# Performance work log

Measured on AMD Instinct MI355X. Metric: run time of the kernel, lower is better.

Reference implementation:

```python
import jax, jax.numpy as jnp
import numpy as np

N, E, IN, H, G, OUT = 50000, 800000, 128, 128, 64, 10
HEADS, C = 4, 32  # per-head dim = H // HEADS so 4-head concat -> H (keeps chain dims consistent)


def setup_inputs() -> dict:
    key = jax.random.key(0)
    ks = jax.random.split(key, 16)
    p = lambda i, shape: jax.random.normal(ks[i], shape, jnp.float32) * 0.05
    return {
        "x": jax.random.normal(ks[0], (N, IN), jnp.float32),
        "edge_index": jax.random.randint(ks[1], (2, E), 0, N),
        "batch": jnp.sort(jax.random.randint(ks[2], (N,), 0, G)),
        "gcn_W": p(3, (IN, H)), "gcn_b": jnp.zeros((H,), jnp.float32),
        "gat_W": p(4, (H, HEADS * C)),
        "att_src": p(5, (HEADS, C)), "att_dst": p(6, (HEADS, C)),
        "gat_b": jnp.zeros((HEADS * C,), jnp.float32),
        "ec_W1": p(7, (2 * H, 128)), "ec_b1": jnp.zeros((128,), jnp.float32),
        "ec_W2": p(8, (128, H)), "ec_b2": jnp.zeros((H,), jnp.float32),
        "gin_W1": p(9, (H, 128)), "gin_b1": jnp.zeros((128,), jnp.float32),
        "gin_W2": p(10, (128, H)), "gin_b2": jnp.zeros((H,), jnp.float32),
        "gate_W1": p(11, (H, 128)), "gate_b1": jnp.zeros((128,), jnp.float32),
        "gate_W2": p(12, (128, 1)), "gate_b2": jnp.zeros((1,), jnp.float32),
        "fc_W": p(13, (H, OUT)), "fc_b": jnp.zeros((OUT,), jnp.float32),
    }


def reference(x, edge_index, batch, gcn_W, gcn_b, gat_W, att_src, att_dst, gat_b,
              ec_W1, ec_b1, ec_W2, ec_b2, gin_W1, gin_b1, gin_W2, gin_b2,
              gate_W1, gate_b1, gate_W2, gate_b2, fc_W, fc_b):
    src, dst = edge_index[0], edge_index[1]
    loop = jnp.arange(N)
    src_l = jnp.concatenate([src, loop])  # self loops for GCN / GAT
    dst_l = jnp.concatenate([dst, loop])

    deg = jax.ops.segment_sum(jnp.ones_like(dst_l, jnp.float32), dst_l, N)
    dinv = jnp.where(deg > 0, jax.lax.rsqrt(deg), 0.0)
    h = x @ gcn_W
    norm = dinv[src_l] * dinv[dst_l]  # [E+N]
    h = jax.ops.segment_sum(h[src_l] * norm[:, None], dst_l, N) + gcn_b
    h = jax.nn.relu(h)

    # ---- GATConv: 4 heads, per-target edge softmax, concat ----
    g = (h @ gat_W).reshape(N, HEADS, C)
    a_src = (g * att_src).sum(-1)  # [N, HEADS]
    a_dst = (g * att_dst).sum(-1)
    e = jax.nn.leaky_relu(a_src[src_l] + a_dst[dst_l], 0.2)  # [E+N, HEADS]
    e_max = jax.ops.segment_max(e, dst_l, N)
    e = jnp.exp(e - e_max[dst_l])
    e_sum = jax.ops.segment_sum(e, dst_l, N)
    alpha = e / (e_sum[dst_l] + 1e-16)
    h = jax.ops.segment_sum(g[src_l] * alpha[..., None], dst_l, N).reshape(N, HEADS * C) + gat_b
    h = jax.nn.elu(h)

    # ---- EdgeConv: nn([x_i, x_j - x_i]) with max aggregation ----
    msg = jnp.concatenate([h[dst], h[src] - h[dst]], axis=-1)  # [E, 2H]
    msg = jax.nn.relu(msg @ ec_W1 + ec_b1) @ ec_W2 + ec_b2
    agg = jax.ops.segment_max(msg, dst, N)
    h = jax.nn.relu(jnp.where(jnp.isfinite(agg), agg, 0.0))  # isolated nodes -> 0 (PyG scatter-max fill)

    # ---- GINConv (eps=0): nn(x + sum_j x_j) ----
    s = h + jax.ops.segment_sum(h[src], dst, N)
    h = jax.nn.relu(jax.nn.relu(s @ gin_W1 + gin_b1) @ gin_W2 + gin_b2)

    # ---- GlobalAttention pooling: per-graph softmax gating ----
    gate = jax.nn.relu(h @ gate_W1 + gate_b1) @ gate_W2 + gate_b2  # [N, 1]
    gmax = jax.ops.segment_max(gate, batch, G)
    ge = jnp.exp(gate - gmax[batch])
    gsum = jax.ops.segment_sum(ge, batch, G)
    w = ge / (gsum[batch] + 1e-16)
    pooled = jax.ops.segment_sum(w * h, batch, G)  # [G, H]

    out = pooled @ fc_W + fc_b
    return jax.nn.log_softmax(out, axis=1)
```

## Files before the change

### kernel.cpp

```cpp
#include <hip/hip_runtime.h>

#define H 128
#define OUTD 10

typedef short bf16x8 __attribute__((ext_vector_type(8)));
typedef float f32x4 __attribute__((ext_vector_type(4)));

__device__ __forceinline__ unsigned short f2bf(float x) {
  unsigned u = __float_as_uint(x);
  u += 0x7fffu + ((u >> 16) & 1u);
  return (unsigned short)(u >> 16);
}
__device__ __forceinline__ unsigned pack2bf(float a, float b) {
  return (unsigned)f2bf(a) | ((unsigned)f2bf(b) << 16);
}
__device__ __forceinline__ float bf2f(unsigned short u) {
  return __uint_as_float(((unsigned)u) << 16);
}
__device__ __forceinline__ float bflo(unsigned u) { return __uint_as_float(u << 16); }
__device__ __forceinline__ float bfhi(unsigned u) { return __uint_as_float(u & 0xffff0000u); }

__global__ void prep_w(const float* __restrict__ gcnW, const float* __restrict__ gatW,
                       const float* __restrict__ ecW1, const float* __restrict__ ecW2,
                       const float* __restrict__ ginW1, const float* __restrict__ ginW2,
                       const float* __restrict__ gtW1, unsigned short* __restrict__ WT) {
  int f = blockIdx.x * 256 + threadIdx.x;
  if (f >= 8 * 16384) return;
  int m = f >> 14, idx = f & 16383;
  int j = idx >> 7, k = idx & 127;
  int src = k * 128 + j;
  float v;
  switch (m) {
    case 0: v = gcnW[src]; break;
    case 1: v = gatW[src]; break;
    case 2: v = ecW1[src] - ecW1[16384 + src]; break;
    case 3: v = ecW1[16384 + src]; break;
    case 4: v = ecW2[src]; break;
    case 5: v = ginW1[src]; break;
    case 6: v = ginW2[src]; break;
    default: v = gtW1[src]; break;
  }
  WT[f] = f2bf(v);
}

template <int IN_BF, int RELU, int BIAS>
__global__ __launch_bounds__(256) void dense_mfma(const void* __restrict__ Xv,
                                                  const unsigned short* __restrict__ WT,
                                                  const float* __restrict__ bias,
                                                  unsigned short* __restrict__ Y, int n) {
  __shared__ unsigned short tile[64][136];
  const int tid = threadIdx.x, lane = tid & 63, wave = tid >> 6;
  const int jl = lane & 15, kg = lane >> 4;
  const int base = blockIdx.x * 64;
  if (base >= n) return;
  const int nr = min(64, n - base);
  if (IN_BF) {
    const uint4* X4 = (const uint4*)Xv;
#pragma unroll
    for (int it = 0; it < 4; ++it) {
      int f = it * 256 + tid, r = f >> 4, q = f & 15;
      if (r < nr) *(uint4*)&tile[r][q * 8] = X4[(size_t)(base + r) * 16 + q];
    }
  } else {
    const float* X = (const float*)Xv;
#pragma unroll
    for (int it = 0; it < 16; ++it) {
      int f = it * 256 + tid, r = f >> 6, kp = f & 63;
      if (r < nr) {
        float2 v = *(const float2*)&X[(size_t)(base + r) * H + 2 * kp];
        *(unsigned*)&tile[r][2 * kp] = pack2bf(v.x, v.y);
      }
    }
  }
  __syncthreads();
  bf16x8 afrag[4];
#pragma unroll
  for (int kk = 0; kk < 4; ++kk)
    afrag[kk] = *(const bf16x8*)&tile[wave * 16 + jl][kk * 32 + kg * 8];
  f32x4 acc[8];
#pragma unroll
  for (int jt = 0; jt < 8; ++jt) {
    f32x4 c = {0.f, 0.f, 0.f, 0.f};
#pragma unroll
    for (int kk = 0; kk < 4; ++kk) {
      bf16x8 bf = *(const bf16x8*)&WT[(size_t)(jt * 16 + jl) * H + kk * 32 + kg * 8];
      c = __builtin_amdgcn_mfma_f32_16x16x32_bf16(afrag[kk], bf, c, 0, 0, 0);
    }
    if (BIAS) {
      float bb = bias[jt * 16 + jl];
#pragma unroll
      for (int r = 0; r < 4; ++r) c[r] += bb;
    }
    if (RELU) {
#pragma unroll
      for (int r = 0; r < 4; ++r) c[r] = fmaxf(c[r], 0.f);
    }
    acc[jt] = c;
  }
  __syncthreads();
#pragma unroll
  for (int jt = 0; jt < 8; ++jt)
#pragma unroll
    for (int r = 0; r < 4; ++r) tile[wave * 16 + kg * 4 + r][jt * 16 + jl] = f2bf(acc[jt][r]);
  __syncthreads();
#pragma unroll
  for (int it = 0; it < 4; ++it) {
    int f = it * 256 + tid, r = f >> 4, q = f & 15;
    if (r < nr) *(uint4*)&Y[(size_t)(base + r) * H + q * 8] = *(const uint4*)&tile[r][q * 8];
  }
}

__global__ __launch_bounds__(256) void dense_dual(const unsigned short* __restrict__ X,
                                                  const unsigned short* __restrict__ WT1,
                                                  const unsigned short* __restrict__ WT2,
                                                  const float* __restrict__ bias2,
                                                  unsigned short* __restrict__ Y1,
                                                  unsigned short* __restrict__ Y2, int n) {
  __shared__ unsigned short tile[64][136];
  const int tid = threadIdx.x, lane = tid & 63, wave = tid >> 6;
  const int jl = lane & 15, kg = lane >> 4;
  const int base = blockIdx.x * 64;
  if (base >= n) return;
  const int nr = min(64, n - base);
  const uint4* X4 = (const uint4*)X;
#pragma unroll
  for (int it = 0; it < 4; ++it) {
    int f = it * 256 + tid, r = f >> 4, q = f & 15;
    if (r < nr) *(uint4*)&tile[r][q * 8] = X4[(size_t)(base + r) * 16 + q];
  }
  __syncthreads();
  bf16x8 afrag[4];
#pragma unroll
  for (int kk = 0; kk < 4; ++kk)
    afrag[kk] = *(const bf16x8*)&tile[wave * 16 + jl][kk * 32 + kg * 8];
  f32x4 acc[8];
#pragma unroll
  for (int jt = 0; jt < 8; ++jt) {
    f32x4 c = {0.f, 0.f, 0.f, 0.f};
#pragma unroll
    for (int kk = 0; kk < 4; ++kk) {
      bf16x8 bf = *(const bf16x8*)&WT1[(size_t)(jt * 16 + jl) * H + kk * 32 + kg * 8];
      c = __builtin_amdgcn_mfma_f32_16x16x32_bf16(afrag[kk], bf, c, 0, 0, 0);
    }
    acc[jt] = c;
  }
  __syncthreads();
#pragma unroll
  for (int jt = 0; jt < 8; ++jt)
#pragma unroll
    for (int r = 0; r < 4; ++r) tile[wave * 16 + kg * 4 + r][jt * 16 + jl] = f2bf(acc[jt][r]);
  __syncthreads();
#pragma unroll
  for (int it = 0; it < 4; ++it) {
    int f = it * 256 + tid, r = f >> 4, q = f & 15;
    if (r < nr) *(uint4*)&Y1[(size_t)(base + r) * H + q * 8] = *(const uint4*)&tile[r][q * 8];
  }
  __syncthreads();
#pragma unroll
  for (int jt = 0; jt < 8; ++jt) {
    f32x4 c = {0.f, 0.f, 0.f, 0.f};
#pragma unroll
    for (int kk = 0; kk < 4; ++kk) {
      bf16x8 bf = *(const bf16x8*)&WT2[(size_t)(jt * 16 + jl) * H + kk * 32 + kg * 8];
      c = __builtin_amdgcn_mfma_f32_16x16x32_bf16(afrag[kk], bf, c, 0, 0, 0);
    }
    float bb = bias2[jt * 16 + jl];
#pragma unroll
    for (int r = 0; r < 4; ++r) c[r] += bb;
    acc[jt] = c;
  }
  __syncthreads();
#pragma unroll
  for (int jt = 0; jt < 8; ++jt)
#pragma unroll
    for (int r = 0; r < 4; ++r) tile[wave * 16 + kg * 4 + r][jt * 16 + jl] = f2bf(acc[jt][r]);
  __syncthreads();
#pragma unroll
  for (int it = 0; it < 4; ++it) {
    int f = it * 256 + tid, r = f >> 4, q = f & 15;
    if (r < nr) *(uint4*)&Y2[(size_t)(base + r) * H + q * 8] = *(const uint4*)&tile[r][q * 8];
  }
}

__global__ void zero_int(int* p, int n) {
  int i = blockIdx.x * 256 + threadIdx.x;
  if (i < n) p[i] = 0;
}
__global__ void csr_count(const int* __restrict__ ei, int* __restrict__ cnt, int E) {
  int e = blockIdx.x * 256 + threadIdx.x;
  if (e < E) atomicAdd(&cnt[ei[(size_t)E + e]], 1);
}
__global__ __launch_bounds__(1024) void scan50k(const int* __restrict__ cnt,
                                                int* __restrict__ row_ptr, int n) {
  __shared__ int ls[1024];
  int t = threadIdx.x;
  int chunk = (n + 1023) >> 10;
  int a = t * chunk;
  if (a > n) a = n;
  int b = a + chunk;
  if (b > n) b = n;
  int s = 0;
  for (int i = a; i < b; ++i) s += cnt[i];
  ls[t] = s;
  __syncthreads();
  for (int off = 1; off < 1024; off <<= 1) {
    int v = (t >= off) ? ls[t - off] : 0;
    __syncthreads();
    ls[t] += v;
    __syncthreads();
  }
  int run = (t > 0) ? ls[t - 1] : 0;
  for (int i = a; i < b; ++i) {
    row_ptr[i] = run;
    run += cnt[i];
  }
  if (t == 1023) row_ptr[n] = ls[1023];
}
__global__ void copy_int(const int* __restrict__ a, int* __restrict__ b, int n) {
  int i = blockIdx.x * 256 + threadIdx.x;
  if (i < n) b[i] = a[i];
}
__global__ void csr_fill(const int* __restrict__ ei, int* __restrict__ cursor,
                         int* __restrict__ csr_src, int E) {
  int e = blockIdx.x * 256 + threadIdx.x;
  if (e >= E) return;
  int s = ei[e], d = ei[(size_t)E + e];
  int p = atomicAdd(&cursor[d], 1);
  csr_src[p] = s;
}
__global__ void dinv_kernel(const int* __restrict__ row_ptr, float* __restrict__ dinv, int n) {
  int i = blockIdx.x * 256 + threadIdx.x;
  if (i < n) dinv[i] = rsqrtf((float)(1 + row_ptr[i + 1] - row_ptr[i]));
}

__global__ __launch_bounds__(256) void gcn_gather(const unsigned short* __restrict__ h,
                                                  const float* __restrict__ dinv,
                                                  const int* __restrict__ row_ptr,
                                                  const int* __restrict__ csr_src,
                                                  const float* __restrict__ bias,
                                                  unsigned short* __restrict__ out, int n) {
  int node = blockIdx.x * 4 + (threadIdx.x >> 6);
  int lane = threadIdx.x & 63;
  if (node >= n) return;
  const unsigned* hu = (const unsigned*)h;
  float di = dinv[node];
  unsigned v = hu[(size_t)node * 64 + lane];
  float t0 = bflo(v) * di, t1 = bfhi(v) * di;
  int a = row_ptr[node], b = row_ptr[node + 1];
  int e = a;
  for (; e + 4 <= b; e += 4) {
    int s0 = csr_src[e], s1 = csr_src[e + 1], s2 = csr_src[e + 2], s3 = csr_src[e + 3];
    unsigned w0 = hu[(size_t)s0 * 64 + lane], w1 = hu[(size_t)s1 * 64 + lane];
    unsigned w2 = hu[(size_t)s2 * 64 + lane], w3 = hu[(size_t)s3 * 64 + lane];
    float d0 = dinv[s0], d1 = dinv[s1], d2 = dinv[s2], d3 = dinv[s3];
    t0 = fmaf(bflo(w0), d0, t0);
    t1 = fmaf(bfhi(w0), d0, t1);
    t0 = fmaf(bflo(w1), d1, t0);
    t1 = fmaf(bfhi(w1), d1, t1);
    t0 = fmaf(bflo(w2), d2, t0);
    t1 = fmaf(bfhi(w2), d2, t1);
    t0 = fmaf(bflo(w3), d3, t0);
    t1 = fmaf(bfhi(w3), d3, t1);
  }
  for (; e < b; ++e) {
    int s = csr_src[e];
    float ds = dinv[s];
    unsigned w = hu[(size_t)s * 64 + lane];
    t0 = fmaf(bflo(w), ds, t0);
    t1 = fmaf(bfhi(w), ds, t1);
  }
  float y0 = fmaxf(fmaf(t0, di, bias[lane * 2]), 0.f);
  float y1 = fmaxf(fmaf(t1, di, bias[lane * 2 + 1]), 0.f);
  ((unsigned*)out)[(size_t)node * 64 + lane] = pack2bf(y0, y1);
}

__global__ void att_pre(const unsigned short* __restrict__ g, const float* __restrict__ attS,
                        const float* __restrict__ attD, float* __restrict__ asrc,
                        float* __restrict__ adst, int n) {
  int t = blockIdx.x * 256 + threadIdx.x;
  if (t >= n * 4) return;
  int i = t >> 2, hd = t & 3;
  const unsigned* gr = (const unsigned*)(g + (size_t)i * H + hd * 32);
  float s1 = 0.f, s2 = 0.f;
#pragma unroll
  for (int p = 0; p < 16; ++p) {
    unsigned u = gr[p];
    float a = bflo(u), b = bfhi(u);
    s1 = fmaf(a, attS[hd * 32 + 2 * p], fmaf(b, attS[hd * 32 + 2 * p + 1], s1));
    s2 = fmaf(a, attD[hd * 32 + 2 * p], fmaf(b, attD[hd * 32 + 2 * p + 1], s2));
  }
  asrc[t] = s1;
  adst[t] = s2;
}

__device__ __forceinline__ float lrelu_exp(float v) {
  v = v > 0.f ? v : 0.2f * v;
  return __expf(v);
}

__global__ __launch_bounds__(256) void gat_gather(const unsigned short* __restrict__ g,
                                                  const float* __restrict__ asrc,
                                                  const float* __restrict__ adst,
                                                  const int* __restrict__ row_ptr,
                                                  const int* __restrict__ csr_src,
                                                  const float* __restrict__ bias,
                                                  unsigned short* __restrict__ out, int n) {
  int node = blockIdx.x * 4 + (threadIdx.x >> 6);
  int lane = threadIdx.x & 63;
  if (node >= n) return;
  const int hd = lane >> 4;
  const unsigned* gu = (const unsigned*)g;
  float adc = adst[node * 4 + hd];
  float w = lrelu_exp(asrc[node * 4 + hd] + adc);
  unsigned u = gu[(size_t)node * 64 + lane];
  float acc0 = w * bflo(u), acc1 = w * bfhi(u), wsum = w;
  int a = row_ptr[node], b = row_ptr[node + 1];
  int e = a;
  for (; e + 4 <= b; e += 4) {
    int s0 = csr_src[e], s1 = csr_src[e + 1], s2 = csr_src[e + 2], s3 = csr_src[e + 3];
    unsigned u0 = gu[(size_t)s0 * 64 + lane], u1 = gu[(size_t)s1 * 64 + lane];
    unsigned u2 = gu[(size_t)s2 * 64 + lane], u3 = gu[(size_t)s3 * 64 + lane];
    float w0 = lrelu_exp(asrc[s0 * 4 + hd] + adc), w1 = lrelu_exp(asrc[s1 * 4 + hd] + adc);
    float w2 = lrelu_exp(asrc[s2 * 4 + hd] + adc), w3 = lrelu_exp(asrc[s3 * 4 + hd] + adc);
    acc0 = fmaf(w0, bflo(u0), acc0);
    acc1 = fmaf(w0, bfhi(u0), acc1);
    acc0 = fmaf(w1, bflo(u1), acc0);
    acc1 = fmaf(w1, bfhi(u1), acc1);
    acc0 = fmaf(w2, bflo(u2), acc0);
    acc1 = fmaf(w2, bfhi(u2), acc1);
    acc0 = fmaf(w3, bflo(u3), acc0);
    acc1 = fmaf(w3, bfhi(u3), acc1);
    wsum += w0 + w1 + w2 + w3;
  }
  for (; e < b; ++e) {
    int s = csr_src[e];
    unsigned us = gu[(size_t)s * 64 + lane];
    float we = lrelu_exp(asrc[s * 4 + hd] + adc);
    acc0 = fmaf(we, bflo(us), acc0);
    acc1 = fmaf(we, bfhi(us), acc1);
    wsum += we;
  }
  float inv = 1.f / (wsum + 1e-16f);
  float r0 = acc0 * inv + bias[2 * lane];
  float r1 = acc1 * inv + bias[2 * lane + 1];
  r0 = r0 > 0.f ? r0 : expm1f(r0);
  r1 = r1 > 0.f ? r1 : expm1f(r1);
  ((unsigned*)out)[(size_t)node * 64 + lane] = pack2bf(r0, r1);
}

__global__ __launch_bounds__(256) void edgeconv_node(const unsigned short* __restrict__ A,
                                                     const unsigned short* __restrict__ Bm,
                                                     const int* __restrict__ row_ptr,
                                                     const int* __restrict__ csr_src,
                                                     const unsigned short* __restrict__ W2T,
                                                     const float* __restrict__ b2,
                                                     unsigned short* __restrict__ out, int n) {
  int node = blockIdx.x * 4 + (threadIdx.x >> 6);
  if (node >= n) return;
  const int lane = threadIdx.x & 63;
  const int jl = lane & 15, kg = lane >> 4;
  int a = row_ptr[node], b = row_ptr[node + 1];
  unsigned* orow = (unsigned*)(out + (size_t)node * H);
  if (a == b) {
    if (kg == 0 && !(jl & 1)) {
#pragma unroll
      for (int jt = 0; jt < 8; ++jt) orow[jt * 8 + (jl >> 1)] = 0u;
    }
    return;
  }
  bf16x8 ad[4];
  const unsigned short* Arow = A + (size_t)node * H;
#pragma unroll
  for (int kk = 0; kk < 4; ++kk) ad[kk] = *(const bf16x8*)&Arow[kk * 32 + kg * 8];
  f32x4 best[8];
#pragma unroll
  for (int jt = 0; jt < 8; ++jt) best[jt] = {-1e30f, -1e30f, -1e30f, -1e30f};
  for (int base = a; base < b; base += 16) {
    const int m = min(16, b - base);
    bf16x8 af[4];
    if (jl < m) {
      int s = csr_src[base + jl];
      const unsigned short* Brow = Bm + (size_t)s * H;
#pragma unroll
      for (int kk = 0; kk < 4; ++kk) {
        bf16x8 bv = *(const bf16x8*)&Brow[kk * 32 + kg * 8];
        bf16x8 o;
#pragma unroll
        for (int q = 0; q < 8; ++q) {
          float xv = bf2f((unsigned short)ad[kk][q]) + bf2f((unsigned short)bv[q]);
          o[q] = (short)f2bf(fmaxf(xv, 0.f));
        }
        af[kk] = o;
      }
    } else {
#pragma unroll
      for (int kk = 0; kk < 4; ++kk) {
#pragma unroll
        for (int q = 0; q < 8; ++q) af[kk][q] = 0;
      }
    }
#pragma unroll
    for (int jt = 0; jt < 8; ++jt) {
      f32x4 c = {0.f, 0.f, 0.f, 0.f};
#pragma unroll
      for (int kk = 0; kk < 4; ++kk) {
        bf16x8 wf = *(const bf16x8*)&W2T[(size_t)(jt * 16 + jl) * H + kk * 32 + kg * 8];
        c = __builtin_amdgcn_mfma_f32_16x16x32_bf16(af[kk], wf, c, 0, 0, 0);
      }
#pragma unroll
      for (int r = 0; r < 4; ++r) {
        int row = kg * 4 + r;
        best[jt][r] = fmaxf(best[jt][r], (row < m) ? c[r] : -1e30f);
      }
    }
  }
#pragma unroll
  for (int jt = 0; jt < 8; ++jt) {
    float mv = fmaxf(fmaxf(best[jt][0], best[jt][1]), fmaxf(best[jt][2], best[jt][3]));
    mv = fmaxf(mv, __shfl_xor(mv, 16));
    mv = fmaxf(mv, __shfl_xor(mv, 32));
    float val = fmaxf(mv + b2[jt * 16 + jl], 0.f);
    float other = __shfl_xor(val, 1);
    if (kg == 0 && !(jl & 1)) orow[jt * 8 + (jl >> 1)] = pack2bf(val, other);
  }
}

__global__ __launch_bounds__(256) void gin_gather(const unsigned short* __restrict__ h,
                                                  const int* __restrict__ row_ptr,
                                                  const int* __restrict__ csr_src,
                                                  unsigned short* __restrict__ out, int n) {
  int node = blockIdx.x * 4 + (threadIdx.x >> 6);
  int lane = threadIdx.x & 63;
  if (node >= n) return;
  const unsigned* hu = (const unsigned*)h;
  unsigned v = hu[(size_t)node * 64 + lane];
  float t0 = bflo(v), t1 = bfhi(v);
  int a = row_ptr[node], b = row_ptr[node + 1];
  int e = a;
  for (; e + 4 <= b; e += 4) {
    int s0 = csr_src[e], s1 = csr_src[e + 1], s2 = csr_src[e + 2], s3 = csr_src[e + 3];
    unsigned w0 = hu[(size_t)s0 * 64 + lane], w1 = hu[(size_t)s1 * 64 + lane];
    unsigned w2 = hu[(size_t)s2 * 64 + lane], w3 = hu[(size_t)s3 * 64 + lane];
    t0 += bflo(w0) + bflo(w1) + bflo(w2) + bflo(w3);
    t1 += bfhi(w0) + bfhi(w1) + bfhi(w2) + bfhi(w3);
  }
  for (; e < b; ++e) {
    int s = csr_src[e];
    unsigned w = hu[(size_t)s * 64 + lane];
    t0 += bflo(w);
    t1 += bfhi(w);
  }
  ((unsigned*)out)[(size_t)node * 64 + lane] = pack2bf(t0, t1);
}

__global__ __launch_bounds__(256) void gate_dot(const unsigned short* __restrict__ X,
                                                const float* __restrict__ w2,
                                                const float* __restrict__ b2,
                                                float* __restrict__ gate, int n) {
  int wid = (blockIdx.x * 256 + threadIdx.x) >> 6;
  int lane = threadIdx.x & 63;
  if (wid >= n) return;
  unsigned u = ((const unsigned*)X)[(size_t)wid * 64 + lane];
  float a = fmaf(bflo(u), w2[lane * 2], bfhi(u) * w2[lane * 2 + 1]);
#pragma unroll
  for (int off = 32; off; off >>= 1) a += __shfl_xor(a, off);
  if (lane == 0) gate[wid] = a + b2[0];
}
__global__ void starts_kernel(const int* __restrict__ batch, int* __restrict__ starts, int n,
                              int G) {
  int i = blockIdx.x * 256 + threadIdx.x;
  if (i >= n) return;
  int b = batch[i];
  int bp = (i == 0) ? -1 : batch[i - 1];
  for (int g = bp + 1; g <= b; ++g) starts[g] = i;
  if (i == n - 1)
    for (int g = b + 1; g <= G; ++g) starts[g] = n;
}
__global__ __launch_bounds__(256) void pool_fused(float* __restrict__ gate,
                                                  const unsigned short* __restrict__ h4,
                                                  const int* __restrict__ starts,
                                                  const float* __restrict__ fcW,
                                                  const float* __restrict__ fcB,
                                                  float* __restrict__ out) {
  __shared__ float red[256];
  __shared__ float pl[128];
  int g = blockIdx.x, t = threadIdx.x;
  int s0 = starts[g], s1 = starts[g + 1];
  float m = -1e30f;
  for (int i = s0 + t; i < s1; i += 256) m = fmaxf(m, gate[i]);
  red[t] = m;
  __syncthreads();
  for (int off = 128; off; off >>= 1) {
    if (t < off) red[t] = fmaxf(red[t], red[t + off]);
    __syncthreads();
  }
  m = red[0];
  __syncthreads();
  float sm = 0.f;
  for (int i = s0 + t; i < s1; i += 256) {
    float ge = __expf(gate[i] - m);
    gate[i] = ge;
    sm += ge;
  }
  red[t] = sm;
  __syncthreads();
  for (int off = 128; off; off >>= 1) {
    if (t < off) red[t] += red[t + off];
    __syncthreads();
  }
  float inv = 1.f / (red[0] + 1e-16f);
  __syncthreads();
  int c = t & 127, half = t >> 7;
  float acc = 0.f;
  for (int i = s0 + half; i < s1; i += 2) acc = fmaf(gate[i], bf2f(h4[(size_t)i * H + c]), acc);
  red[t] = acc;
  __syncthreads();
  if (t < 128) pl[t] = (red[t] + red[t + 128]) * inv;
  __syncthreads();
  if (t < OUTD) {
    float o = fcB[t];
    for (int k = 0; k < 128; ++k) o = fmaf(pl[k], fcW[k * OUTD + t], o);
    red[t] = o;
  }
  __syncthreads();
  if (t == 0) {
    float mm = -1e30f;
    for (int j = 0; j < OUTD; ++j) mm = fmaxf(mm, red[j]);
    float s = 0.f;
    for (int j = 0; j < OUTD; ++j) s += __expf(red[j] - mm);
    float l = logf(s);
    for (int j = 0; j < OUTD; ++j) out[g * OUTD + j] = red[j] - mm - l;
  }
}

extern "C" void kernel_launch(void* const* d_in, const int* in_sizes, int n_in, void* d_out,
                              int out_size, void* d_ws, size_t ws_size, hipStream_t stream) {
  const float* x = (const float*)d_in[0];
  const int* ei = (const int*)d_in[1];
  const int* batch = (const int*)d_in[2];
  const float* gcnW = (const float*)d_in[3];
  const float* gcnB = (const float*)d_in[4];
  const float* gatW = (const float*)d_in[5];
  const float* attS = (const float*)d_in[6];
  const float* attD = (const float*)d_in[7];
  const float* gatB = (const float*)d_in[8];
  const float* ecW1 = (const float*)d_in[9];
  const float* ecB1 = (const float*)d_in[10];
  const float* ecW2 = (const float*)d_in[11];
  const float* ecB2 = (const float*)d_in[12];
  const float* ginW1 = (const float*)d_in[13];
  const float* ginB1 = (const float*)d_in[14];
  const float* ginW2 = (const float*)d_in[15];
  const float* ginB2 = (const float*)d_in[16];
  const float* gtW1 = (const float*)d_in[17];
  const float* gtB1 = (const float*)d_in[18];
  const float* gtW2 = (const float*)d_in[19];
  const float* gtB2 = (const float*)d_in[20];
  const float* fcW = (const float*)d_in[21];
  const float* fcB = (const float*)d_in[22];

  const int N = in_sizes[0] / H;
  const int E = in_sizes[1] / 2;
  const int G = out_size / OUTD;
  const size_t NH = (size_t)N * H;

  auto align16 = [](char* p) { return (char*)(((uintptr_t)p + 15) & ~(uintptr_t)15); };
  char* p = (char*)d_ws;
  float* dinv = (float*)p;           p += (size_t)N * 4;
  float* asrc = (float*)p;           p += (size_t)4 * N * 4;
  float* adst = (float*)p;           p += (size_t)4 * N * 4;
  float* gate = (float*)p;           p += (size_t)N * 4;
  int* starts = (int*)p;             p += (size_t)(G + 1) * 4;
  int* cnt = (int*)p;                p += (size_t)N * 4;
  int* row_ptr = (int*)p;            p += (size_t)(N + 1) * 4;
  int* cursor = (int*)p;             p += (size_t)N * 4;
  int* csr_src = (int*)p;            p += (size_t)E * 4;
  p = align16(p);
  unsigned short* WT = (unsigned short*)p;  p += (size_t)8 * 16384 * 2;
  p = align16(p);
  unsigned short* T0 = (unsigned short*)p;  p += NH * 2;
  p = align16(p);
  unsigned short* T1 = (unsigned short*)p;  p += NH * 2;
  p = align16(p);
  unsigned short* T2 = (unsigned short*)p;  p += NH * 2;
  p = align16(p);
  unsigned short* T3 = (unsigned short*)p;  p += NH * 2;

  const unsigned short* gcnT = WT;
  const unsigned short* gatT = WT + 16384;
  const unsigned short* WaT = WT + 2 * 16384;
  const unsigned short* WbT = WT + 3 * 16384;
  const unsigned short* W2T = WT + 4 * 16384;
  const unsigned short* gin1T = WT + 5 * 16384;
  const unsigned short* gin2T = WT + 6 * 16384;
  const unsigned short* gt1T = WT + 7 * 16384;

  const int gN = (N + 255) / 256;
  const int gE = (E + 255) / 256;
  const int gDense = (N + 63) / 64;
  const int gW4 = (N + 3) / 4;

  prep_w<<<(8 * 16384 + 255) / 256, 256, 0, stream>>>(gcnW, gatW, ecW1, ecW2, ginW1, ginW2,
                                                      gtW1, WT);
  zero_int<<<gN, 256, 0, stream>>>(cnt, N);
  csr_count<<<gE, 256, 0, stream>>>(ei, cnt, E);
  scan50k<<<1, 1024, 0, stream>>>(cnt, row_ptr, N);
  copy_int<<<gN, 256, 0, stream>>>(row_ptr, cursor, N);
  csr_fill<<<gE, 256, 0, stream>>>(ei, cursor, csr_src, E);
  dinv_kernel<<<gN, 256, 0, stream>>>(row_ptr, dinv, N);

  dense_mfma<0, 0, 0><<<gDense, 256, 0, stream>>>(x, gcnT, nullptr, T0, N);
  gcn_gather<<<gW4, 256, 0, stream>>>(T0, dinv, row_ptr, csr_src, gcnB, T1, N);

  dense_mfma<1, 0, 0><<<gDense, 256, 0, stream>>>(T1, gatT, nullptr, T2, N);
  att_pre<<<(N * 4 + 255) / 256, 256, 0, stream>>>(T2, attS, attD, asrc, adst, N);
  gat_gather<<<gW4, 256, 0, stream>>>(T2, asrc, adst, row_ptr, csr_src, gatB, T0, N);

  dense_dual<<<gDense, 256, 0, stream>>>(T0, WaT, WbT, ecB1, T1, T2, N);
  edgeconv_node<<<gW4, 256, 0, stream>>>(T1, T2, row_ptr, csr_src, W2T, ecB2, T3, N);

  gin_gather<<<gW4, 256, 0, stream>>>(T3, row_ptr, csr_src, T0, N);
  dense_mfma<1, 1, 1><<<gDense, 256, 0, stream>>>(T0, gin1T, ginB1, T1, N);
  dense_mfma<1, 1, 1><<<gDense, 256, 0, stream>>>(T1, gin2T, ginB2, T2, N);

  dense_mfma<1, 1, 1><<<gDense, 256, 0, stream>>>(T2, gt1T, gtB1, T0, N);
  gate_dot<<<(N * 64 + 255) / 256, 256, 0, stream>>>(T0, gtW2, gtB2, gate, N);
  starts_kernel<<<gN, 256, 0, stream>>>(batch, starts, N, G);
  pool_fused<<<G, 256, 0, stream>>>(gate, T2, starts, fcW, fcB, (float*)d_out);
}
```

Baseline: 976.0 us.

## Edge-tiled EdgeConv with atomic max, fuse GIN MLP and gate head

EdgeConv changes from per-node wave processing, which leaves MFMA tiles partly idle for low-degree nodes, to dense 64-edge tiles in CSR order. Tiles are double-buffered in a persistent grid, and results are merged with atomicMax on an order-preserving uint32 encoding into an fp32 buffer. The GIN two-layer MLP is fused into one kernel, and the gate's first layer is fused with its dot product. The GCN gather is also unrolled to 8 edges. The cost is extra atomic traffic, a fill pass, a csr_dst array and a wider fp32 intermediate. Isolated nodes now decode the fill value to 0, so the output should match the reference.

Result: faster. 817.0 us (-16.3%).

```diff
diff --git a/kernel.cpp b/kernel.cpp
--- a/kernel.cpp
+++ b/kernel.cpp
@@ -19,6 +19,15 @@
 }
 __device__ __forceinline__ float bflo(unsigned u) { return __uint_as_float(u << 16); }
 __device__ __forceinline__ float bfhi(unsigned u) { return __uint_as_float(u & 0xffff0000u); }
+
+__device__ __forceinline__ unsigned fenc(float x) {
+  unsigned u = __float_as_uint(x);
+  return (u & 0x80000000u) ? ~u : (u | 0x80000000u);
+}
+__device__ __forceinline__ float fdec(unsigned u) {
+  u = (u & 0x80000000u) ? (u & 0x7fffffffu) : ~u;
+  return __uint_as_float(u);
+}
 
 __global__ void prep_w(const float* __restrict__ gcnW, const float* __restrict__ gatW,
                        const float* __restrict__ ecW1, const float* __restrict__ ecW2,
@@ -182,6 +191,131 @@
   }
 }
 
+__global__ __launch_bounds__(256) void dense_chain(const unsigned short* __restrict__ X,
+                                                   const unsigned short* __restrict__ WT1,
+                                                   const float* __restrict__ b1,
+                                                   const unsigned short* __restrict__ WT2,
+                                                   const float* __restrict__ b2,
+                                                   unsigned short* __restrict__ Y, int n) {
+  __shared__ unsigned short tile[64][136];
+  const int tid = threadIdx.x, lane = tid & 63, wave = tid >> 6;
+  const int jl = lane & 15, kg = lane >> 4;
+  const int base = blockIdx.x * 64;
+  if (base >= n) return;
+  const int nr = min(64, n - base);
+  const uint4* X4 = (const uint4*)X;
+#pragma unroll
+  for (int it = 0; it < 4; ++it) {
+    int f = it * 256 + tid, r = f >> 4, q = f & 15;
+    if (r < nr) *(uint4*)&tile[r][q * 8] = X4[(size_t)(base + r) * 16 + q];
+  }
+  __syncthreads();
+  bf16x8 af[4];
+#pragma unroll
+  for (int kk = 0; kk < 4; ++kk) af[kk] = *(const bf16x8*)&tile[wave * 16 + jl][kk * 32 + kg * 8];
+  f32x4 acc[8];
+#pragma unroll
+  for (int jt = 0; jt < 8; ++jt) {
+    f32x4 c = {0.f, 0.f, 0.f, 0.f};
+#pragma unroll
+    for (int kk = 0; kk < 4; ++kk) {
+      bf16x8 bf = *(const bf16x8*)&WT1[(size_t)(jt * 16 + jl) * H + kk * 32 + kg * 8];
+      c = __builtin_amdgcn_mfma_f32_16x16x32_bf16(af[kk], bf, c, 0, 0, 0);
+    }
+    float bb = b1[jt * 16 + jl];
+#pragma unroll
+    for (int r = 0; r < 4; ++r) c[r] = fmaxf(c[r] + bb, 0.f);
+    acc[jt] = c;
+  }
+  __syncthreads();
+#pragma unroll
+  for (int jt = 0; jt < 8; ++jt)
+#pragma unroll
+    for (int r = 0; r < 4; ++r) tile[wave * 16 + kg * 4 + r][jt * 16 + jl] = f2bf(acc[jt][r]);
+  __syncthreads();
+#pragma unroll
+  for (int kk = 0; kk < 4; ++kk) af[kk] = *(const bf16x8*)&tile[wave * 16 + jl][kk * 32 + kg * 8];
+#pragma unroll
+  for (int jt = 0; jt < 8; ++jt) {
+    f32x4 c = {0.f, 0.f, 0.f, 0.f};
+#pragma unroll
+    for (int kk = 0; kk < 4; ++kk) {
+      bf16x8 bf = *(const bf16x8*)&WT2[(size_t)(jt * 16 + jl) * H + kk * 32 + kg * 8];
+      c = __builtin_amdgcn_mfma_f32_16x16x32_bf16(af[kk], bf, c, 0, 0, 0);
+    }
+    float bb = b2[jt * 16 + jl];
+#pragma unroll
+    for (int r = 0; r < 4; ++r) c[r] = fmaxf(c[r] + bb, 0.f);
+    acc[jt] = c;
+  }
+  __syncthreads();
+#pragma unroll
+  for (int jt = 0; jt < 8; ++jt)
+#pragma unroll
+    for (int r = 0; r < 4; ++r) tile[wave * 16 + kg * 4 + r][jt * 16 + jl] = f2bf(acc[jt][r]);
+  __syncthreads();
+#pragma unroll
+  for (int it = 0; it < 4; ++it) {
+    int f = it * 256 + tid, r = f >> 4, q = f & 15;
+    if (r < nr) *(uint4*)&Y[(size_t)(base + r) * H + q * 8] = *(const uint4*)&tile[r][q * 8];
+  }
+}
+
+__global__ __launch_bounds__(256) void dense_gate(const unsigned short* __restrict__ X,
+                                                  const unsigned short* __restrict__ WT,
+                                                  const float* __restrict__ b1,
+                                                  const float* __restrict__ w2,
+                                                  const float* __restrict__ b2,
+                                                  float* __restrict__ gate, int n) {
+  __shared__ unsigned short tile[64][136];
+  const int tid = threadIdx.x, lane = tid & 63, wave = tid >> 6;
+  const int jl = lane & 15, kg = lane >> 4;
+  const int base = blockIdx.x * 64;
+  if (base >= n) return;
+  const int nr = min(64, n - base);
+  const uint4* X4 = (const uint4*)X;
+#pragma unroll
+  for (int it = 0; it < 4; ++it) {
+    int f = it * 256 + tid, r = f >> 4, q = f & 15;
+    if (r < nr) *(uint4*)&tile[r][q * 8] = X4[(size_t)(base + r) * 16 + q];
+  }
+  __syncthreads();
+  bf16x8 af[4];
+#pragma unroll
+  for (int kk = 0; kk < 4; ++kk) af[kk] = *(const bf16x8*)&tile[wave * 16 + jl][kk * 32 + kg * 8];
+  float p0 = 0.f, p1 = 0.f, p2 = 0.f, p3 = 0.f;
+#pragma unroll
+  for (int jt = 0; jt < 8; ++jt) {
+    f32x4 c = {0.f, 0.f, 0.f, 0.f};
+#pragma unroll
+    for (int kk = 0; kk < 4; ++kk) {
+      bf16x8 bf = *(const bf16x8*)&WT[(size_t)(jt * 16 + jl) * H + kk * 32 + kg * 8];
+      c = __builtin_amdgcn_mfma_f32_16x16x32_bf16(af[kk], bf, c, 0, 0, 0);
+    }
+    float bb = b1[jt * 16 + jl];
+    float wv = w2[jt * 16 + jl];
+    p0 = fmaf(fmaxf(c[0] + bb, 0.f), wv, p0);
+    p1 = fmaf(fmaxf(c[1] + bb, 0.f), wv, p1);
+    p2 = fmaf(fmaxf(c[2] + bb, 0.f), wv, p2);
+    p3 = fmaf(fmaxf(c[3] + bb, 0.f), wv, p3);
+  }
+#pragma unroll
+  for (int off = 1; off <= 8; off <<= 1) {
+    p0 += __shfl_xor(p0, off);
+    p1 += __shfl_xor(p1, off);
+    p2 += __shfl_xor(p2, off);
+    p3 += __shfl_xor(p3, off);
+  }
+  if (jl == 0) {
+    float bb2 = b2[0];
+    int row = wave * 16 + kg * 4;
+    if (row + 0 < nr) gate[base + row + 0] = p0 + bb2;
+    if (row + 1 < nr) gate[base + row + 1] = p1 + bb2;
+    if (row + 2 < nr) gate[base + row + 2] = p2 + bb2;
+    if (row + 3 < nr) gate[base + row + 3] = p3 + bb2;
+  }
+}
+
 __global__ void zero_int(int* p, int n) {
   int i = blockIdx.x * 256 + threadIdx.x;
   if (i < n) p[i] = 0;
@@ -221,16 +355,21 @@
   if (i < n) b[i] = a[i];
 }
 __global__ void csr_fill(const int* __restrict__ ei, int* __restrict__ cursor,
-                         int* __restrict__ csr_src, int E) {
+                         int* __restrict__ csr_src, int* __restrict__ csr_dst, int E) {
   int e = blockIdx.x * 256 + threadIdx.x;
   if (e >= E) return;
   int s = ei[e], d = ei[(size_t)E + e];
   int p = atomicAdd(&cursor[d], 1);
   csr_src[p] = s;
+  csr_dst[p] = d;
 }
 __global__ void dinv_kernel(const int* __restrict__ row_ptr, float* __restrict__ dinv, int n) {
   int i = blockIdx.x * 256 + threadIdx.x;
   if (i < n) dinv[i] = rsqrtf((float)(1 + row_ptr[i + 1] - row_ptr[i]));
+}
+__global__ void fill_u32(unsigned* p, unsigned v, size_t n) {
+  size_t i = (size_t)blockIdx.x * 256 + threadIdx.x;
+  if (i < n) p[i] = v;
 }
 
 __global__ __launch_bounds__(256) void gcn_gather(const unsigned short* __restrict__ h,
@@ -248,19 +387,21 @@
   float t0 = bflo(v) * di, t1 = bfhi(v) * di;
   int a = row_ptr[node], b = row_ptr[node + 1];
   int e = a;
-  for (; e + 4 <= b; e += 4) {
-    int s0 = csr_src[e], s1 = csr_src[e + 1], s2 = csr_src[e + 2], s3 = csr_src[e + 3];
-    unsigned w0 = hu[(size_t)s0 * 64 + lane], w1 = hu[(size_t)s1 * 64 + lane];
-    unsigned w2 = hu[(size_t)s2 * 64 + lane], w3 = hu[(size_t)s3 * 64 + lane];
-    float d0 = dinv[s0], d1 = dinv[s1], d2 = dinv[s2], d3 = dinv[s3];
-    t0 = fmaf(bflo(w0), d0, t0);
-    t1 = fmaf(bfhi(w0), d0, t1);
-    t0 = fmaf(bflo(w1), d1, t0);
-    t1 = fmaf(bfhi(w1), d1, t1);
-    t0 = fmaf(bflo(w2), d2, t0);
-    t1 = fmaf(bfhi(w2), d2, t1);
-    t0 = fmaf(bflo(w3), d3, t0);
-    t1 = fmaf(bfhi(w3), d3, t1);
+  for (; e + 8 <= b; e += 8) {
+    int sx[8];
+#pragma unroll
+    for (int i = 0; i < 8; ++i) sx[i] = csr_src[e + i];
+    unsigned w[8];
+    float dd[8];
+#pragma unroll
+    for (int i = 0; i < 8; ++i) w[i] = hu[(size_t)sx[i] * 64 + lane];
+#pragma unroll
+    for (int i = 0; i < 8; ++i) dd[i] = dinv[sx[i]];
+#pragma unroll
+    for (int i = 0; i < 8; ++i) {
+      t0 = fmaf(bflo(w[i]), dd[i], t0);
+      t1 = fmaf(bfhi(w[i]), dd[i], t1);
+    }
   }
   for (; e < b; ++e) {
     int s = csr_src[e];
@@ -348,57 +489,81 @@
   ((unsigned*)out)[(size_t)node * 64 + lane] = pack2bf(r0, r1);
 }
 
-__global__ __launch_bounds__(256) void edgeconv_node(const unsigned short* __restrict__ A,
+__global__ __launch_bounds__(256) void edgeconv_tile(const unsigned short* __restrict__ A,
                                                      const unsigned short* __restrict__ Bm,
-                                                     const int* __restrict__ row_ptr,
                                                      const int* __restrict__ csr_src,
+                                                     const int* __restrict__ csr_dst,
                                                      const unsigned short* __restrict__ W2T,
                                                      const float* __restrict__ b2,
-                                                     unsigned short* __restrict__ out, int n) {
-  int node = blockIdx.x * 4 + (threadIdx.x >> 6);
-  if (node >= n) return;
-  const int lane = threadIdx.x & 63;
+                                                     unsigned* __restrict__ hec, int E) {
+  __shared__ unsigned short buf[2][64][136];
+  __shared__ int dbuf[2][64];
+  const int tid = threadIdx.x, lane = tid & 63, wave = tid >> 6;
   const int jl = lane & 15, kg = lane >> 4;
-  int a = row_ptr[node], b = row_ptr[node + 1];
-  unsigned* orow = (unsigned*)(out + (size_t)node * H);
-  if (a == b) {
-    if (kg == 0 && !(jl & 1)) {
-#pragma unroll
-      for (int jt = 0; jt < 8; ++jt) orow[jt * 8 + (jl >> 1)] = 0u;
-    }
-    return;
-  }
-  bf16x8 ad[4];
-  const unsigned short* Arow = A + (size_t)node * H;
-#pragma unroll
-  for (int kk = 0; kk < 4; ++kk) ad[kk] = *(const bf16x8*)&Arow[kk * 32 + kg * 8];
-  f32x4 best[8];
-#pragma unroll
-  for (int jt = 0; jt < 8; ++jt) best[jt] = {-1e30f, -1e30f, -1e30f, -1e30f};
-  for (int base = a; base < b; base += 16) {
-    const int m = min(16, b - base);
-    bf16x8 af[4];
-    if (jl < m) {
-      int s = csr_src[base + jl];
-      const unsigned short* Brow = Bm + (size_t)s * H;
-#pragma unroll
-      for (int kk = 0; kk < 4; ++kk) {
-        bf16x8 bv = *(const bf16x8*)&Brow[kk * 32 + kg * 8];
-        bf16x8 o;
-#pragma unroll
-        for (int q = 0; q < 8; ++q) {
-          float xv = bf2f((unsigned short)ad[kk][q]) + bf2f((unsigned short)bv[q]);
-          o[q] = (short)f2bf(fmaxf(xv, 0.f));
-        }
-        af[kk] = o;
+  const int srow = tid >> 2, sq = tid & 3;
+  float b2v[8];
+#pragma unroll
+  for (int jt = 0; jt < 8; ++jt) b2v[jt] = b2[jt * 16 + jl];
+
+  const int tiles = (E + 63) >> 6;
+  int t = blockIdx.x;
+  if (t >= tiles) return;
+  int cur = 0;
+  {
+    int base = t << 6;
+    int ne = min(64, E - base);
+    uint2 pk[8];
+    if (srow < ne) {
+      int d = csr_dst[base + srow], s = csr_src[base + srow];
+      const uint2* Ar = (const uint2*)(A + (size_t)d * H + sq * 32);
+      const uint2* Br = (const uint2*)(Bm + (size_t)s * H + sq * 32);
+#pragma unroll
+      for (int i = 0; i < 8; ++i) {
+        uint2 va = Ar[i], vb = Br[i];
+        pk[i].x = pack2bf(fmaxf(bflo(va.x) + bflo(vb.x), 0.f), fmaxf(bfhi(va.x) + bfhi(vb.x), 0.f));
+        pk[i].y = pack2bf(fmaxf(bflo(va.y) + bflo(vb.y), 0.f), fmaxf(bfhi(va.y) + bfhi(vb.y), 0.f));
       }
     } else {
 #pragma unroll
-      for (int kk = 0; kk < 4; ++kk) {
-#pragma unroll
-        for (int q = 0; q < 8; ++q) af[kk][q] = 0;
+      for (int i = 0; i < 8; ++i) pk[i] = {0u, 0u};
+    }
+#pragma unroll
+    for (int i = 0; i < 8; ++i) *(uint2*)&buf[0][srow][sq * 32 + i * 4] = pk[i];
+    if (sq == 0) dbuf[0][srow] = (srow < ne) ? csr_dst[base + srow] : -1;
+  }
+  __syncthreads();
+
+  for (; t < tiles; t += gridDim.x) {
+    const int nt = t + gridDim.x;
+    const bool havenext = nt < tiles;
+    uint2 pk[8];
+    if (havenext) {
+      int base = nt << 6;
+      int ne = min(64, E - base);
+      if (srow < ne) {
+        int d = csr_dst[base + srow], s = csr_src[base + srow];
+        const uint2* Ar = (const uint2*)(A + (size_t)d * H + sq * 32);
+        const uint2* Br = (const uint2*)(Bm + (size_t)s * H + sq * 32);
+#pragma unroll
+        for (int i = 0; i < 8; ++i) {
+          uint2 va = Ar[i], vb = Br[i];
+          pk[i].x =
+              pack2bf(fmaxf(bflo(va.x) + bflo(vb.x), 0.f), fmaxf(bfhi(va.x) + bfhi(vb.x), 0.f));
+          pk[i].y =
+              pack2bf(fmaxf(bflo(va.y) + bflo(vb.y), 0.f), fmaxf(bfhi(va.y) + bfhi(vb.y), 0.f));
+        }
+      } else {
+#pragma unroll
+        for (int i = 0; i < 8; ++i) pk[i] = {0u, 0u};
       }
     }
+    bf16x8 af[4];
+#pragma unroll
+    for (int kk = 0; kk < 4; ++kk)
+      af[kk] = *(const bf16x8*)&buf[cur][wave * 16 + jl][kk * 32 + kg * 8];
+    const int r0 = wave * 16 + kg * 4;
+    const int d0 = dbuf[cur][r0 + 0], d1 = dbuf[cur][r0 + 1];
+    const int d2 = dbuf[cur][r0 + 2], d3 = dbuf[cur][r0 + 3];
 #pragma unroll
     for (int jt = 0; jt < 8; ++jt) {
       f32x4 c = {0.f, 0.f, 0.f, 0.f};
@@ -407,65 +572,70 @@
         bf16x8 wf = *(const bf16x8*)&W2T[(size_t)(jt * 16 + jl) * H + kk * 32 + kg * 8];
         c = __builtin_amdgcn_mfma_f32_16x16x32_bf16(af[kk], wf, c, 0, 0, 0);
       }
-#pragma unroll
-      for (int r = 0; r < 4; ++r) {
-        int row = kg * 4 + r;
-        best[jt][r] = fmaxf(best[jt][r], (row < m) ? c[r] : -1e30f);
-      }
-    }
-  }
-#pragma unroll
-  for (int jt = 0; jt < 8; ++jt) {
-    float mv = fmaxf(fmaxf(best[jt][0], best[jt][1]), fmaxf(best[jt][2], best[jt][3]));
-    mv = fmaxf(mv, __shfl_xor(mv, 16));
-    mv = fmaxf(mv, __shfl_xor(mv, 32));
-    float val = fmaxf(mv + b2[jt * 16 + jl], 0.f);
-    float other = __shfl_xor(val, 1);
-    if (kg == 0 && !(jl & 1)) orow[jt * 8 + (jl >> 1)] = pack2bf(val, other);
-  }
-}
-
-__global__ __launch_bounds__(256) void gin_gather(const unsigned short* __restrict__ h,
+      const int col = jt * 16 + jl;
+      int cd = d0;
+      float m = c[0];
+      if (d1 != cd) {
+        if (cd >= 0) atomicMax(&hec[(size_t)cd * H + col], fenc(m + b2v[jt]));
+        cd = d1;
+        m = c[1];
+      } else
+        m = fmaxf(m, c[1]);
+      if (d2 != cd) {
+        if (cd >= 0) atomicMax(&hec[(size_t)cd * H + col], fenc(m + b2v[jt]));
+        cd = d2;
+        m = c[2];
+      } else
+        m = fmaxf(m, c[2]);
+      if (d3 != cd) {
+        if (cd >= 0) atomicMax(&hec[(size_t)cd * H + col], fenc(m + b2v[jt]));
+        cd = d3;
+        m = c[3];
+      } else
+        m = fmaxf(m, c[3]);
+      if (cd >= 0) atomicMax(&hec[(size_t)cd * H + col], fenc(m + b2v[jt]));
+    }
+    if (havenext) {
+      int base = nt << 6;
+      int ne = min(64, E - base);
+#pragma unroll
+      for (int i = 0; i < 8; ++i) *(uint2*)&buf[cur ^ 1][srow][sq * 32 + i * 4] = pk[i];
+      if (sq == 0) dbuf[cur ^ 1][srow] = (srow < ne) ? csr_dst[base + srow] : -1;
+    }
+    __syncthreads();
+    cur ^= 1;
+  }
+}
+
+__global__ __launch_bounds__(256) void gin_gather(const unsigned* __restrict__ hec,
                                                   const int* __restrict__ row_ptr,
                                                   const int* __restrict__ csr_src,
                                                   unsigned short* __restrict__ out, int n) {
   int node = blockIdx.x * 4 + (threadIdx.x >> 6);
   int lane = threadIdx.x & 63;
   if (node >= n) return;
-  const unsigned* hu = (const unsigned*)h;
-  unsigned v = hu[(size_t)node * 64 + lane];
-  float t0 = bflo(v), t1 = bfhi(v);
+  uint2 v = *(const uint2*)&hec[(size_t)node * H + lane * 2];
+  float t0 = fdec(v.x), t1 = fdec(v.y);
   int a = row_ptr[node], b = row_ptr[node + 1];
   int e = a;
   for (; e + 4 <= b; e += 4) {
     int s0 = csr_src[e], s1 = csr_src[e + 1], s2 = csr_src[e + 2], s3 = csr_src[e + 3];
-    unsigned w0 = hu[(size_t)s0 * 64 + lane], w1 = hu[(size_t)s1 * 64 + lane];
-    unsigned w2 = hu[(size_t)s2 * 64 + lane], w3 = hu[(size_t)s3 * 64 + lane];
-    t0 += bflo(w0) + bflo(w1) + bflo(w2) + bflo(w3);
-    t1 += bfhi(w0) + bfhi(w1) + bfhi(w2) + bfhi(w3);
+    uint2 w0 = *(const uint2*)&hec[(size_t)s0 * H + lane * 2];
+    uint2 w1 = *(const uint2*)&hec[(size_t)s1 * H + lane * 2];
+    uint2 w2 = *(const uint2*)&hec[(size_t)s2 * H + lane * 2];
+    uint2 w3 = *(const uint2*)&hec[(size_t)s3 * H + lane * 2];
+    t0 += fdec(w0.x) + fdec(w1.x) + fdec(w2.x) + fdec(w3.x);
+    t1 += fdec(w0.y) + fdec(w1.y) + fdec(w2.y) + fdec(w3.y);
   }
   for (; e < b; ++e) {
     int s = csr_src[e];
-    unsigned w = hu[(size_t)s * 64 + lane];
-    t0 += bflo(w);
-    t1 += bfhi(w);
+    uint2 w = *(const uint2*)&hec[(size_t)s * H + lane * 2];
+    t0 += fdec(w.x);
+    t1 += fdec(w.y);
   }
   ((unsigned*)out)[(size_t)node * 64 + lane] = pack2bf(t0, t1);
 }
 
-__global__ __launch_bounds__(256) void gate_dot(const unsigned short* __restrict__ X,
-                                                const float* __restrict__ w2,
-                                                const float* __restrict__ b2,
-                                                float* __restrict__ gate, int n) {
-  int wid = (blockIdx.x * 256 + threadIdx.x) >> 6;
-  int lane = threadIdx.x & 63;
-  if (wid >= n) return;
-  unsigned u = ((const unsigned*)X)[(size_t)wid * 64 + lane];
-  float a = fmaf(bflo(u), w2[lane * 2], bfhi(u) * w2[lane * 2 + 1]);
-#pragma unroll
-  for (int off = 32; off; off >>= 1) a += __shfl_xor(a, off);
-  if (lane == 0) gate[wid] = a + b2[0];
-}
 __global__ void starts_kernel(const int* __restrict__ batch, int* __restrict__ starts, int n,
                               int G) {
   int i = blockIdx.x * 256 + threadIdx.x;
@@ -566,6 +736,7 @@
 
   auto align16 = [](char* p) { return (char*)(((uintptr_t)p + 15) & ~(uintptr_t)15); };
   char* p = (char*)d_ws;
+  unsigned* hec = (unsigned*)p;      p += NH * 4;
   float* dinv = (float*)p;           p += (size_t)N * 4;
   float* asrc = (float*)p;           p += (size_t)4 * N * 4;
   float* adst = (float*)p;           p += (size_t)4 * N * 4;
@@ -575,6 +746,7 @@
   int* row_ptr = (int*)p;            p += (size_t)(N + 1) * 4;
   int* cursor = (int*)p;             p += (size_t)N * 4;
   int* csr_src = (int*)p;            p += (size_t)E * 4;
+  int* csr_dst = (int*)p;            p += (size_t)E * 4;
   p = align16(p);
   unsigned short* WT = (unsigned short*)p;  p += (size_t)8 * 16384 * 2;
   p = align16(p);
@@ -583,8 +755,6 @@
   unsigned short* T1 = (unsigned short*)p;  p += NH * 2;
   p = align16(p);
   unsigned short* T2 = (unsigned short*)p;  p += NH * 2;
-  p = align16(p);
-  unsigned short* T3 = (unsigned short*)p;  p += NH * 2;
 
   const unsigned short* gcnT = WT;
   const unsigned short* gatT = WT + 16384;
@@ -596,6 +766,7 @@
   const unsigned short* gt1T = WT + 7 * 16384;
 
   const int gN = (N + 255) / 256;
+  const int gNH = (int)((NH + 255) / 256);
   const int gE = (E + 255) / 256;
   const int gDense = (N + 63) / 64;
   const int gW4 = (N + 3) / 4;
@@ -606,7 +777,7 @@
   csr_count<<<gE, 256, 0, stream>>>(ei, cnt, E);
   scan50k<<<1, 1024, 0, stream>>>(cnt, row_ptr, N);
   copy_int<<<gN, 256, 0, stream>>>(row_ptr, cursor, N);
-  csr_fill<<<gE, 256, 0, stream>>>(ei, cursor, csr_src, E);
+  csr_fill<<<gE, 256, 0, stream>>>(ei, cursor, csr_src, csr_dst, E);
   dinv_kernel<<<gN, 256, 0, stream>>>(row_ptr, dinv, N);
 
   dense_mfma<0, 0, 0><<<gDense, 256, 0, stream>>>(x, gcnT, nullptr, T0, N);
@@ -617,14 +788,13 @@
   gat_gather<<<gW4, 256, 0, stream>>>(T2, asrc, adst, row_ptr, csr_src, gatB, T0, N);
 
   dense_dual<<<gDense, 256, 0, stream>>>(T0, WaT, WbT, ecB1, T1, T2, N);
-  edgeconv_node<<<gW4, 256, 0, stream>>>(T1, T2, row_ptr, csr_src, W2T, ecB2, T3, N);
-
-  gin_gather<<<gW4, 256, 0, stream>>>(T3, row_ptr, csr_src, T0, N);
-  dense_mfma<1, 1, 1><<<gDense, 256, 0, stream>>>(T0, gin1T, ginB1, T1, N);
-  dense_mfma<1, 1, 1><<<gDense, 256, 0, stream>>>(T1, gin2T, ginB2, T2, N);
-
-  dense_mfma<1, 1, 1><<<gDense, 256, 0, stream>>>(T2, gt1T, gtB1, T0, N);
-  gate_dot<<<(N * 64 + 255) / 256, 256, 0, stream>>>(T0, gtW2, gtB2, gate, N);
+  fill_u32<<<gNH, 256, 0, stream>>>(hec, 0x80000000u, NH);
+  edgeconv_tile<<<2048, 256, 0, stream>>>(T1, T2, csr_src, csr_dst, W2T, ecB2, hec, E);
+
+  gin_gather<<<gW4, 256, 0, stream>>>(hec, row_ptr, csr_src, T0, N);
+  dense_chain<<<gDense, 256, 0, stream>>>(T0, gin1T, ginB1, gin2T, ginB2, T2, N);
+
+  dense_gate<<<gDense, 256, 0, stream>>>(T2, gt1T, gtB1, gtW2, gtB2, gate, N);
   starts_kernel<<<gN, 256, 0, stream>>>(batch, starts, N, G);
   pool_fused<<<G, 256, 0, stream>>>(gate, T2, starts, fcW, fcB, (float*)d_out);
 }
```
